# Performance work log

Measured on AMD Instinct MI355X. Metric: run time of the kernel, lower is better.

Reference implementation:

```python
import jax, jax.numpy as jnp
import numpy as np

C1, CS = 512, 32
EPS = 1e-5
_HI, _HJ = np.triu_indices(CS, k=1)  # pairwise (i<j) hadamard index pairs, cs_expand = 496


def setup_inputs() -> dict:
    key = jax.random.key(0)
    ks = jax.random.split(key, 9)
    B, H, W = 16, 32, 32
    return dict(
        x=jax.random.normal(ks[0], (B, C1, H, W), jnp.float32),
        fc_w=jax.random.normal(ks[1], (C1, C1), jnp.float32) * 0.05,   # 1x1 conv kernel
        fc_b=jax.random.normal(ks[2], (C1,), jnp.float32) * 0.05,
        bn_gamma=jax.random.normal(ks[3], (C1,), jnp.float32) * 0.1 + 1.0,
        bn_beta=jax.random.normal(ks[4], (C1,), jnp.float32) * 0.1,
        bn_mean=jax.random.normal(ks[5], (C1,), jnp.float32) * 0.1,    # BN running mean
        bn_var=jax.random.uniform(ks[6], (C1,), jnp.float32) + 0.5,    # BN running var (positive)
        eva_w=jax.random.normal(ks[7], (C1, C1), jnp.float32) * 0.05,
        eva_b=jax.random.normal(ks[8], (C1,), jnp.float32) * 0.05,
    )


def reference(x, fc_w, fc_b, bn_gamma, bn_beta, bn_mean, bn_var, eva_w, eva_b):
    hi = jnp.asarray(_HI)
    hj = jnp.asarray(_HJ)
    # 1x1 conv (pointwise GEMM over channels)
    x = jnp.einsum('bchw,oc->bohw', x, fc_w) + fc_b[None, :, None, None]
    # BatchNorm2d, eval mode (running stats)
    scale = bn_gamma / jnp.sqrt(bn_var + EPS)
    x = (x - bn_mean[None, :, None, None]) * scale[None, :, None, None] + bn_beta[None, :, None, None]
    # channel evaluation logits: global avg pool -> linear
    logits = jnp.mean(x, axis=(2, 3)) @ eva_w.T + eva_b  # [B, C1]
    # top-cs channel selection and gather (eval path)
    _, idx = jax.lax.top_k(logits, CS)                    # [B, CS]
    x_sel = jax.vmap(lambda xi, ii: xi[ii])(x, idx)       # [B, CS, H, W]
    # pairwise hadamard expansion: gather-multiply over (i<j) pairs
    prod = x_sel[:, hi] * x_sel[:, hj]                    # [B, cs_expand, H, W]
    # CrossHadaNorm: per-channel standardize with batch stats, affine from
    # cross-products of norm_x affine params gathered via hadamard_i/j
    mean = jnp.mean(prod, axis=(0, 2, 3), keepdims=True)
    var = jnp.var(prod, axis=(0, 2, 3), keepdims=True)
    g = (bn_gamma[hi] * bn_gamma[hj])[None, :, None, None]
    b = (bn_beta[hi] * bn_beta[hj])[None, :, None, None]
    prod = (prod - mean) / jnp.sqrt(var + EPS) * g + b
    return jnp.concatenate([x, prod], axis=1)             # [B, c1 + cs_expand, H, W]
```

## Files before the change

### kernel.cpp

```cpp
#include <hip/hip_runtime.h>
#include <stdint.h>
#include <stddef.h>

#define B_   16
#define C1_  512
#define HW_  1024
#define CS_  32
#define CE_  496
#define CO_  1008

typedef __attribute__((ext_vector_type(8))) short short8;
typedef __attribute__((ext_vector_type(4))) short short4v;
typedef __attribute__((ext_vector_type(4))) float f32x4;

__device__ __forceinline__ short f2bf(float f) {
  unsigned u = __builtin_bit_cast(unsigned, f);
  unsigned r = (u + 0x7fffu + ((u >> 16) & 1u)) >> 16;
  return (short)(unsigned short)r;
}

__device__ __forceinline__ void gload_lds16(const void* g, void* l) {
  __builtin_amdgcn_global_load_lds(
      (const __attribute__((address_space(1))) unsigned int*)g,
      (__attribute__((address_space(3))) unsigned int*)l, 16, 0, 0);
}

__global__ __launch_bounds__(256) void prep_kernel(
    const float* __restrict__ fc_w, const float* __restrict__ fc_b,
    const float* __restrict__ bn_gamma, const float* __restrict__ bn_beta,
    const float* __restrict__ bn_mean, const float* __restrict__ bn_var,
    short* __restrict__ wbf, float* __restrict__ bs, float* __restrict__ bb) {
  int bid = blockIdx.x, tid = threadIdx.x;
  if (bid < 1024) {
    int i = bid * 256 + tid;
    wbf[i] = f2bf(fc_w[i]);
  } else {
    for (int o = tid; o < C1_; o += 256) {
      float s = bn_gamma[o] / sqrtf(bn_var[o] + 1e-5f);
      bs[o] = s;
      bb[o] = (fc_b[o] - bn_mean[o]) * s + bn_beta[o];
    }
  }
}

__global__ __launch_bounds__(256) void transpose_pool(const float* __restrict__ x,
                                                      short* __restrict__ xT,
                                                      float* __restrict__ partial) {
  __shared__ float tile[64][65];
  int bid = blockIdx.x;
  int b = bid >> 7;
  int tt = bid & 127;
  int ct = tt >> 4, pt = tt & 15;
  int c0 = ct * 64, p0 = pt * 64;
  int tid = threadIdx.x;
  int rr = tid >> 4, lc = tid & 15;
  const float* xb = x + (size_t)b * C1_ * HW_;
#pragma unroll
  for (int it = 0; it < 4; ++it) {
    int c = it * 16 + rr;
    int p4 = lc * 4;
    float4 v = *(const float4*)(xb + (size_t)(c0 + c) * HW_ + p0 + p4);
    tile[c][p4+0] = v.x; tile[c][p4+1] = v.y; tile[c][p4+2] = v.z; tile[c][p4+3] = v.w;
    float g = v.x + v.y + v.z + v.w;
    g += __shfl_down(g, 8, 16);
    g += __shfl_down(g, 4, 16);
    g += __shfl_down(g, 2, 16);
    g += __shfl_down(g, 1, 16);
    if (lc == 0) partial[((size_t)b * 16 + pt) * C1_ + c0 + c] = g;
  }
  __syncthreads();
#pragma unroll
  for (int it = 0; it < 4; ++it) {
    int p = it * 16 + rr;
    int c4 = lc * 4;
    short4v o;
    o[0] = f2bf(tile[c4+0][p]);
    o[1] = f2bf(tile[c4+1][p]);
    o[2] = f2bf(tile[c4+2][p]);
    o[3] = f2bf(tile[c4+3][p]);
    *(short4v*)(xT + (size_t)b * HW_ * C1_ + (size_t)(p0 + p) * C1_ + c0 + c4) = o;
  }
}

__global__ __launch_bounds__(64) void fc_pool_kernel(
    const float* __restrict__ partial, const float* __restrict__ fc_w,
    const float* __restrict__ bs, const float* __restrict__ bb,
    float* __restrict__ pb) {
  int b = blockIdx.x >> 3, ot = blockIdx.x & 7;
  int tid = threadIdx.x;
  __shared__ float px[512];
  for (int c = tid; c < 512; c += 64) {
    float s = 0.f;
#pragma unroll
    for (int pt = 0; pt < 16; ++pt) s += partial[((size_t)b * 16 + pt) * C1_ + c];
    px[c] = s * (1.f / 1024.f);
  }
  __syncthreads();
  int o = ot * 64 + tid;
  const float4* wr = (const float4*)(fc_w + (size_t)o * 512);
  float acc = 0.f;
#pragma unroll 8
  for (int q = 0; q < 128; ++q) {
    float4 w = wr[q];
    acc += w.x * px[q*4] + w.y * px[q*4+1] + w.z * px[q*4+2] + w.w * px[q*4+3];
  }
  pb[b * 512 + o] = acc * bs[o] + bb[o];
}

__global__ __launch_bounds__(64) void eva_kernel(
    const float* __restrict__ pb, const float* __restrict__ eva_w,
    const float* __restrict__ eva_b, float* __restrict__ logits) {
  int b = blockIdx.x >> 3, ot = blockIdx.x & 7;
  int tid = threadIdx.x;
  __shared__ float ps[512];
  for (int c = tid; c < 512; c += 64) ps[c] = pb[b * 512 + c];
  __syncthreads();
  int o = ot * 64 + tid;
  const float4* wr = (const float4*)(eva_w + (size_t)o * 512);
  float acc = 0.f;
#pragma unroll 8
  for (int q = 0; q < 128; ++q) {
    float4 w = wr[q];
    acc += w.x * ps[q*4] + w.y * ps[q*4+1] + w.z * ps[q*4+2] + w.w * ps[q*4+3];
  }
  logits[b * 512 + o] = acc + eva_b[o];
}

__global__ __launch_bounds__(64) void topk_kernel(const float* __restrict__ logits,
                                                  int* __restrict__ idx) {
  int b = blockIdx.x, lane = threadIdx.x;
  float v[8];
  int base = lane * 8;
#pragma unroll
  for (int u = 0; u < 8; ++u) v[u] = logits[b * 512 + base + u];
  for (int it = 0; it < CS_; ++it) {
    float bv = v[0]; int bu = 0;
#pragma unroll
    for (int u = 1; u < 8; ++u) if (v[u] > bv) { bv = v[u]; bu = u; }
    int bi = base + bu;
    for (int off = 32; off; off >>= 1) {
      float ov = __shfl_down(bv, off);
      int   oi = __shfl_down(bi, off);
      if (ov > bv || (ov == bv && oi < bi)) { bv = ov; bi = oi; }
    }
    bi = __shfl(bi, 0);
    if (lane == 0) idx[b * CS_ + it] = bi;
#pragma unroll
    for (int u = 0; u < 8; ++u) if (bi == base + u) v[u] = -3.4e38f;
  }
}

__global__ __launch_bounds__(256) void gemm_kernel(const short* __restrict__ W,
                                                   const short* __restrict__ XT,
                                                   const float* __restrict__ bs,
                                                   const float* __restrict__ bb,
                                                   float* __restrict__ out) {
  __shared__ char smem[65536];
  int bid = (blockIdx.x & 7) * 64 + (blockIdx.x >> 3);
  int b = bid >> 5;
  int t = bid & 31;
  int mt = t & 3, ntile = t >> 2;
  int m0 = mt * 128, n0 = ntile * 128;
  const short* Ag = W + (size_t)m0 * 512;
  const short* Bg = XT + (size_t)b * HW_ * 512 + (size_t)n0 * 512;
  int tid = threadIdx.x;
  int lane = tid & 63, wave = tid >> 6;
  int wr = wave >> 1, wc = wave & 1;
  int mrow = wr * 64, ncol = wc * 64;
  int lrow = lane & 15;
  int swz = (lrow & 7) << 4;

  f32x4 acc[4][4];
#pragma unroll
  for (int i = 0; i < 4; ++i)
#pragma unroll
    for (int j = 0; j < 4; ++j) acc[i][j] = (f32x4){0.f, 0.f, 0.f, 0.f};

#define STAGE(dstbase, k0)                                                      \
  {                                                                             \
    _Pragma("unroll")                                                           \
    for (int it_ = 0; it_ < 4; ++it_) {                                         \
      int s_ = it_ * 256 + tid;                                                 \
      int L_ = s_ * 16;                                                         \
      int row_ = L_ >> 7;                                                       \
      int w_ = L_ & 127;                                                        \
      int srcs_ = (w_ ^ ((row_ & 7) << 4)) >> 1;                                \
      gload_lds16(Ag + (size_t)row_ * 512 + (k0) + srcs_,                       \
                  smem + (dstbase) + L_);                                       \
      gload_lds16(Bg + (size_t)row_ * 512 + (k0) + srcs_,                       \
                  smem + 32768 + (dstbase) + L_);                               \
    }                                                                           \
  }

  STAGE(0, 0)
  asm volatile("s_waitcnt vmcnt(0)" ::: "memory");
  __syncthreads();

  int cur = 0;
  for (int kt = 0; kt < 8; ++kt) {
    if (kt < 7) STAGE((cur ^ 1) * 16384, (kt + 1) * 64)
    const char* Ab = smem + cur * 16384;
    const char* Bb = smem + 32768 + cur * 16384;
#pragma unroll
    for (int kk = 0; kk < 2; ++kk) {
      int kb = (kk * 64 + (lane >> 4) * 16) ^ swz;
      short8 af[4], bfv[4];
#pragma unroll
      for (int f = 0; f < 4; ++f) {
        af[f]  = *(const short8*)(Ab + (mrow + f * 16 + lrow) * 128 + kb);
        bfv[f] = *(const short8*)(Bb + (ncol + f * 16 + lrow) * 128 + kb);
      }
#pragma unroll
      for (int mf = 0; mf < 4; ++mf)
#pragma unroll
        for (int nf = 0; nf < 4; ++nf)
          acc[mf][nf] = __builtin_amdgcn_mfma_f32_16x16x32_bf16(af[mf], bfv[nf], acc[mf][nf], 0, 0, 0);
    }
    asm volatile("s_waitcnt vmcnt(0)" ::: "memory");
    __syncthreads();
    cur ^= 1;
  }

  float* outb = out + (size_t)b * CO_ * HW_;
#pragma unroll
  for (int mf = 0; mf < 4; ++mf) {
#pragma unroll
    for (int j = 0; j < 4; ++j) {
      int o = m0 + mrow + mf * 16 + (lane >> 4) * 4 + j;
      float s = bs[o], bv = bb[o];
#pragma unroll
      for (int nf = 0; nf < 4; ++nf) {
        int p = n0 + ncol + nf * 16 + lrow;
        outb[(size_t)o * HW_ + p] = acc[mf][nf][j] * s + bv;
      }
    }
  }
#undef STAGE
}

__global__ __launch_bounds__(256) void hada_kernel(
    const int* __restrict__ idx, const float* __restrict__ bn_gamma,
    const float* __restrict__ bn_beta, float* __restrict__ out) {
  int e = blockIdx.x, tid = threadIdx.x;
  int lane = tid & 63, wave = tid >> 6;
  int i = 0, rem = e;
  while (rem >= 31 - i) { rem -= 31 - i; ++i; }
  int j = i + 1 + rem;

  __shared__ int chi[16], chj[16];
  if (tid < 16) chi[tid] = idx[tid * CS_ + i];
  else if (tid < 32) chj[tid - 16] = idx[(tid - 16) * CS_ + j];
  __syncthreads();

  f32x4 p[16];
  float s = 0.f, s2 = 0.f;
#pragma unroll
  for (int b = 0; b < 16; ++b) {
    const float4* xi = (const float4*)(out + ((size_t)b * CO_ + chi[b]) * HW_);
    const float4* xj = (const float4*)(out + ((size_t)b * CO_ + chj[b]) * HW_);
    float4 a = xi[tid], c = xj[tid];
    p[b][0] = a.x * c.x; p[b][1] = a.y * c.y; p[b][2] = a.z * c.z; p[b][3] = a.w * c.w;
    s  += p[b][0] + p[b][1] + p[b][2] + p[b][3];
    s2 += p[b][0]*p[b][0] + p[b][1]*p[b][1] + p[b][2]*p[b][2] + p[b][3]*p[b][3];
  }
  for (int off = 32; off; off >>= 1) { s += __shfl_down(s, off); s2 += __shfl_down(s2, off); }
  __shared__ float red[8];
  if (lane == 0) { red[wave] = s; red[4 + wave] = s2; }
  __syncthreads();
  float S  = red[0] + red[1] + red[2] + red[3];
  float S2 = red[4] + red[5] + red[6] + red[7];
  float mean = S * (1.f / 16384.f);
  float var  = S2 * (1.f / 16384.f) - mean * mean;
  float sc = (bn_gamma[i] * bn_gamma[j]) / sqrtf(var + 1e-5f);
  float bi_ = bn_beta[i] * bn_beta[j] - mean * sc;

#pragma unroll
  for (int b = 0; b < 16; ++b) {
    float4 r;
    r.x = p[b][0] * sc + bi_;
    r.y = p[b][1] * sc + bi_;
    r.z = p[b][2] * sc + bi_;
    r.w = p[b][3] * sc + bi_;
    ((float4*)(out + ((size_t)b * CO_ + C1_ + e) * HW_))[tid] = r;
  }
}

#define XT_OFF     ((size_t)0)
#define WBF_OFF    ((size_t)16777216)
#define PART_OFF   ((size_t)17301504)
#define PB_OFF     ((size_t)17825792)
#define LOG_OFF    ((size_t)17858560)
#define IDX_OFF    ((size_t)17891328)
#define BS_OFF     ((size_t)17893376)
#define BB_OFF     ((size_t)17895424)

extern "C" void kernel_launch(void* const* d_in, const int* in_sizes, int n_in,
                              void* d_out, int out_size, void* d_ws, size_t ws_size,
                              hipStream_t stream) {
  const float* x        = (const float*)d_in[0];
  const float* fc_w     = (const float*)d_in[1];
  const float* fc_b     = (const float*)d_in[2];
  const float* bn_gamma = (const float*)d_in[3];
  const float* bn_beta  = (const float*)d_in[4];
  const float* bn_mean  = (const float*)d_in[5];
  const float* bn_var   = (const float*)d_in[6];
  const float* eva_w    = (const float*)d_in[7];
  const float* eva_b    = (const float*)d_in[8];
  float* out = (float*)d_out;
  char* ws = (char*)d_ws;

  short* xT      = (short*)(ws + XT_OFF);
  short* wbf     = (short*)(ws + WBF_OFF);
  float* partial = (float*)(ws + PART_OFF);
  float* pb      = (float*)(ws + PB_OFF);
  float* logits  = (float*)(ws + LOG_OFF);
  int*   idx     = (int*)(ws + IDX_OFF);
  float* bs      = (float*)(ws + BS_OFF);
  float* bb      = (float*)(ws + BB_OFF);

  hipLaunchKernelGGL(prep_kernel, dim3(1025), dim3(256), 0, stream,
                     fc_w, fc_b, bn_gamma, bn_beta, bn_mean, bn_var, wbf, bs, bb);
  hipLaunchKernelGGL(transpose_pool, dim3(2048), dim3(256), 0, stream, x, xT, partial);
  hipLaunchKernelGGL(fc_pool_kernel, dim3(128), dim3(64), 0, stream,
                     partial, fc_w, bs, bb, pb);
  hipLaunchKernelGGL(eva_kernel, dim3(128), dim3(64), 0, stream,
                     pb, eva_w, eva_b, logits);
  hipLaunchKernelGGL(topk_kernel, dim3(16), dim3(64), 0, stream, logits, idx);
  hipLaunchKernelGGL(gemm_kernel, dim3(512), dim3(256), 0, stream, wbf, xT, bs, bb, out);
  hipLaunchKernelGGL(hada_kernel, dim3(CE_), dim3(256), 0, stream,
                     idx, bn_gamma, bn_beta, out);
}
```

Measured before the change: 94.97 us.

## Merge prep into transpose kernel and fuse selection stages into cooperative kernel

The weight conversion and BN-constant prep blocks are appended to the transpose/pool grid, removing one launch. The fc-pool, eva linear and top-k kernels are combined into one cooperative kernel separated by grid-wide syncs, replacing three launches with one. This cuts launch gaps between small serial kernels, at the cost of grid.sync overhead and the cooperative-launch requirements.

```diff
diff --git a/kernel.cpp b/kernel.cpp
--- a/kernel.cpp
+++ b/kernel.cpp
@@ -1,6 +1,9 @@
 #include <hip/hip_runtime.h>
+#include <hip/hip_cooperative_groups.h>
 #include <stdint.h>
 #include <stddef.h>
+
+namespace cg = cooperative_groups;
 
 #define B_   16
 #define C1_  512
@@ -25,34 +28,38 @@
       (__attribute__((address_space(3))) unsigned int*)l, 16, 0, 0);
 }
 
-__global__ __launch_bounds__(256) void prep_kernel(
-    const float* __restrict__ fc_w, const float* __restrict__ fc_b,
-    const float* __restrict__ bn_gamma, const float* __restrict__ bn_beta,
-    const float* __restrict__ bn_mean, const float* __restrict__ bn_var,
-    short* __restrict__ wbf, float* __restrict__ bs, float* __restrict__ bb) {
-  int bid = blockIdx.x, tid = threadIdx.x;
-  if (bid < 1024) {
-    int i = bid * 256 + tid;
-    wbf[i] = f2bf(fc_w[i]);
-  } else {
-    for (int o = tid; o < C1_; o += 256) {
-      float s = bn_gamma[o] / sqrtf(bn_var[o] + 1e-5f);
-      bs[o] = s;
-      bb[o] = (fc_b[o] - bn_mean[o]) * s + bn_beta[o];
-    }
-  }
-}
-
 __global__ __launch_bounds__(256) void transpose_pool(const float* __restrict__ x,
                                                       short* __restrict__ xT,
-                                                      float* __restrict__ partial) {
+                                                      float* __restrict__ partial,
+                                                      const float* __restrict__ fc_w,
+                                                      const float* __restrict__ fc_b,
+                                                      const float* __restrict__ bn_gamma,
+                                                      const float* __restrict__ bn_beta,
+                                                      const float* __restrict__ bn_mean,
+                                                      const float* __restrict__ bn_var,
+                                                      short* __restrict__ wbf,
+                                                      float* __restrict__ bs,
+                                                      float* __restrict__ bb) {
+  int bid = blockIdx.x;
+  int tid = threadIdx.x;
+  if (bid >= 2048) {
+    if (bid < 3072) {
+      int i = (bid - 2048) * 256 + tid;
+      wbf[i] = f2bf(fc_w[i]);
+    } else {
+      for (int o = tid; o < C1_; o += 256) {
+        float s = bn_gamma[o] / sqrtf(bn_var[o] + 1e-5f);
+        bs[o] = s;
+        bb[o] = (fc_b[o] - bn_mean[o]) * s + bn_beta[o];
+      }
+    }
+    return;
+  }
   __shared__ float tile[64][65];
-  int bid = blockIdx.x;
   int b = bid >> 7;
   int tt = bid & 127;
   int ct = tt >> 4, pt = tt & 15;
   int c0 = ct * 64, p0 = pt * 64;
-  int tid = threadIdx.x;
   int rr = tid >> 4, lc = tid & 15;
   const float* xb = x + (size_t)b * C1_ * HW_;
 #pragma unroll
@@ -82,71 +89,73 @@
   }
 }
 
-__global__ __launch_bounds__(64) void fc_pool_kernel(
+__global__ __launch_bounds__(64) void select_coop(
     const float* __restrict__ partial, const float* __restrict__ fc_w,
     const float* __restrict__ bs, const float* __restrict__ bb,
-    float* __restrict__ pb) {
+    const float* __restrict__ eva_w, const float* __restrict__ eva_b,
+    float* __restrict__ pb, float* __restrict__ logits, int* __restrict__ idx) {
+  cg::grid_group grid = cg::this_grid();
   int b = blockIdx.x >> 3, ot = blockIdx.x & 7;
   int tid = threadIdx.x;
-  __shared__ float px[512];
-  for (int c = tid; c < 512; c += 64) {
-    float s = 0.f;
-#pragma unroll
-    for (int pt = 0; pt < 16; ++pt) s += partial[((size_t)b * 16 + pt) * C1_ + c];
-    px[c] = s * (1.f / 1024.f);
-  }
-  __syncthreads();
-  int o = ot * 64 + tid;
-  const float4* wr = (const float4*)(fc_w + (size_t)o * 512);
-  float acc = 0.f;
+
+  {
+    __shared__ float px[512];
+    for (int c = tid; c < 512; c += 64) {
+      float s = 0.f;
+#pragma unroll
+      for (int pt = 0; pt < 16; ++pt) s += partial[((size_t)b * 16 + pt) * C1_ + c];
+      px[c] = s * (1.f / 1024.f);
+    }
+    __syncthreads();
+    int o = ot * 64 + tid;
+    const float4* wr = (const float4*)(fc_w + (size_t)o * 512);
+    float acc = 0.f;
 #pragma unroll 8
-  for (int q = 0; q < 128; ++q) {
-    float4 w = wr[q];
-    acc += w.x * px[q*4] + w.y * px[q*4+1] + w.z * px[q*4+2] + w.w * px[q*4+3];
-  }
-  pb[b * 512 + o] = acc * bs[o] + bb[o];
-}
-
-__global__ __launch_bounds__(64) void eva_kernel(
-    const float* __restrict__ pb, const float* __restrict__ eva_w,
-    const float* __restrict__ eva_b, float* __restrict__ logits) {
-  int b = blockIdx.x >> 3, ot = blockIdx.x & 7;
-  int tid = threadIdx.x;
-  __shared__ float ps[512];
-  for (int c = tid; c < 512; c += 64) ps[c] = pb[b * 512 + c];
-  __syncthreads();
-  int o = ot * 64 + tid;
-  const float4* wr = (const float4*)(eva_w + (size_t)o * 512);
-  float acc = 0.f;
+    for (int q = 0; q < 128; ++q) {
+      float4 w = wr[q];
+      acc += w.x * px[q*4] + w.y * px[q*4+1] + w.z * px[q*4+2] + w.w * px[q*4+3];
+    }
+    pb[b * 512 + o] = acc * bs[o] + bb[o];
+  }
+  grid.sync();
+
+  {
+    __shared__ float ps[512];
+    for (int c = tid; c < 512; c += 64) ps[c] = pb[b * 512 + c];
+    __syncthreads();
+    int o = ot * 64 + tid;
+    const float4* wr = (const float4*)(eva_w + (size_t)o * 512);
+    float acc = 0.f;
 #pragma unroll 8
-  for (int q = 0; q < 128; ++q) {
-    float4 w = wr[q];
-    acc += w.x * ps[q*4] + w.y * ps[q*4+1] + w.z * ps[q*4+2] + w.w * ps[q*4+3];
-  }
-  logits[b * 512 + o] = acc + eva_b[o];
-}
-
-__global__ __launch_bounds__(64) void topk_kernel(const float* __restrict__ logits,
-                                                  int* __restrict__ idx) {
-  int b = blockIdx.x, lane = threadIdx.x;
-  float v[8];
-  int base = lane * 8;
-#pragma unroll
-  for (int u = 0; u < 8; ++u) v[u] = logits[b * 512 + base + u];
-  for (int it = 0; it < CS_; ++it) {
-    float bv = v[0]; int bu = 0;
-#pragma unroll
-    for (int u = 1; u < 8; ++u) if (v[u] > bv) { bv = v[u]; bu = u; }
-    int bi = base + bu;
-    for (int off = 32; off; off >>= 1) {
-      float ov = __shfl_down(bv, off);
-      int   oi = __shfl_down(bi, off);
-      if (ov > bv || (ov == bv && oi < bi)) { bv = ov; bi = oi; }
-    }
-    bi = __shfl(bi, 0);
-    if (lane == 0) idx[b * CS_ + it] = bi;
-#pragma unroll
-    for (int u = 0; u < 8; ++u) if (bi == base + u) v[u] = -3.4e38f;
+    for (int q = 0; q < 128; ++q) {
+      float4 w = wr[q];
+      acc += w.x * ps[q*4] + w.y * ps[q*4+1] + w.z * ps[q*4+2] + w.w * ps[q*4+3];
+    }
+    logits[b * 512 + o] = acc + eva_b[o];
+  }
+  grid.sync();
+
+  if (blockIdx.x < 16) {
+    int bb_ = blockIdx.x, lane = tid;
+    float v[8];
+    int base = lane * 8;
+#pragma unroll
+    for (int u = 0; u < 8; ++u) v[u] = logits[bb_ * 512 + base + u];
+    for (int it = 0; it < CS_; ++it) {
+      float bv = v[0]; int bu = 0;
+#pragma unroll
+      for (int u = 1; u < 8; ++u) if (v[u] > bv) { bv = v[u]; bu = u; }
+      int bi = base + bu;
+      for (int off = 32; off; off >>= 1) {
+        float ov = __shfl_down(bv, off);
+        int   oi = __shfl_down(bi, off);
+        if (ov > bv || (ov == bv && oi < bi)) { bv = ov; bi = oi; }
+      }
+      bi = __shfl(bi, 0);
+      if (lane == 0) idx[bb_ * CS_ + it] = bi;
+#pragma unroll
+      for (int u = 0; u < 8; ++u) if (bi == base + u) v[u] = -3.4e38f;
+    }
   }
 }
 
@@ -318,14 +327,18 @@
   float* bs      = (float*)(ws + BS_OFF);
   float* bb      = (float*)(ws + BB_OFF);
 
-  hipLaunchKernelGGL(prep_kernel, dim3(1025), dim3(256), 0, stream,
-                     fc_w, fc_b, bn_gamma, bn_beta, bn_mean, bn_var, wbf, bs, bb);
-  hipLaunchKernelGGL(transpose_pool, dim3(2048), dim3(256), 0, stream, x, xT, partial);
-  hipLaunchKernelGGL(fc_pool_kernel, dim3(128), dim3(64), 0, stream,
-                     partial, fc_w, bs, bb, pb);
-  hipLaunchKernelGGL(eva_kernel, dim3(128), dim3(64), 0, stream,
-                     pb, eva_w, eva_b, logits);
-  hipLaunchKernelGGL(topk_kernel, dim3(16), dim3(64), 0, stream, logits, idx);
+  hipLaunchKernelGGL(transpose_pool, dim3(3073), dim3(256), 0, stream,
+                     x, xT, partial, fc_w, fc_b, bn_gamma, bn_beta, bn_mean, bn_var,
+                     wbf, bs, bb);
+
+  {
+    void* args[9] = {(void*)&partial, (void*)&fc_w, (void*)&bs, (void*)&bb,
+                     (void*)&eva_w, (void*)&eva_b, (void*)&pb, (void*)&logits,
+                     (void*)&idx};
+    hipLaunchCooperativeKernel((const void*)select_coop, dim3(128), dim3(64),
+                               args, 0, stream);
+  }
+
   hipLaunchKernelGGL(gemm_kernel, dim3(512), dim3(256), 0, stream, wbf, xT, bs, bb, out);
   hipLaunchKernelGGL(hada_kernel, dim3(CE_), dim3(256), 0, stream,
                      idx, bn_gamma, bn_beta, out);
```

Result: slower. 121.6 us (+28.0%).

## Fuse transpose/bf16 conversion and pooling into GEMM reading fp32 x directly

Applied to the files above, without the earlier changes.

Removes the separate transpose_pool kernel and its bf16 xT workspace. The GEMM now streams fp32 x tiles (channel-major) into swizzled LDS, converts them to bf16 while building the MFMA B fragments, and computes the spatial pooling partial sums in the mt==0 blocks. It also moves to a 3-buffer, K=32 software pipeline with split vmcnt waits. This saves a full read/write pass over x, at the cost of scalar LDS reads and conversion work inside the inner loop, plus an extra pooling load on one quarter of the blocks.

```diff
diff --git a/kernel.cpp b/kernel.cpp
--- a/kernel.cpp
+++ b/kernel.cpp
@@ -1,4 +1,5 @@
 #include <hip/hip_runtime.h>
+#include <hip/hip_bf16.h>
 #include <stdint.h>
 #include <stddef.h>
 
@@ -10,7 +11,6 @@
 #define CO_  1008
 
 typedef __attribute__((ext_vector_type(8))) short short8;
-typedef __attribute__((ext_vector_type(4))) short short4v;
 typedef __attribute__((ext_vector_type(4))) float f32x4;
 
 __device__ __forceinline__ short f2bf(float f) {
@@ -43,43 +43,132 @@
   }
 }
 
-__global__ __launch_bounds__(256) void transpose_pool(const float* __restrict__ x,
-                                                      short* __restrict__ xT,
-                                                      float* __restrict__ partial) {
-  __shared__ float tile[64][65];
-  int bid = blockIdx.x;
-  int b = bid >> 7;
-  int tt = bid & 127;
-  int ct = tt >> 4, pt = tt & 15;
-  int c0 = ct * 64, p0 = pt * 64;
+__global__ __launch_bounds__(256) void gemm_kernel(const short* __restrict__ W,
+                                                   const float* __restrict__ X,
+                                                   const float* __restrict__ bs,
+                                                   const float* __restrict__ bb,
+                                                   float* __restrict__ out,
+                                                   float* __restrict__ partial) {
+  __shared__ char smem[73728];
+  __shared__ float pool_lds[512];
+  int bid = (blockIdx.x & 7) * 64 + (blockIdx.x >> 3);
+  int b = bid >> 5;
+  int t = bid & 31;
+  int mt = t & 3, ntile = t >> 2;
+  int m0 = mt * 128, n0 = ntile * 128;
+  const short* Ag = W + (size_t)m0 * 512;
+  const float* Xb = X + (size_t)b * C1_ * HW_;
   int tid = threadIdx.x;
-  int rr = tid >> 4, lc = tid & 15;
-  const float* xb = x + (size_t)b * C1_ * HW_;
-#pragma unroll
-  for (int it = 0; it < 4; ++it) {
-    int c = it * 16 + rr;
-    int p4 = lc * 4;
-    float4 v = *(const float4*)(xb + (size_t)(c0 + c) * HW_ + p0 + p4);
-    tile[c][p4+0] = v.x; tile[c][p4+1] = v.y; tile[c][p4+2] = v.z; tile[c][p4+3] = v.w;
-    float g = v.x + v.y + v.z + v.w;
-    g += __shfl_down(g, 8, 16);
-    g += __shfl_down(g, 4, 16);
-    g += __shfl_down(g, 2, 16);
-    g += __shfl_down(g, 1, 16);
-    if (lc == 0) partial[((size_t)b * 16 + pt) * C1_ + c0 + c] = g;
-  }
-  __syncthreads();
-#pragma unroll
-  for (int it = 0; it < 4; ++it) {
-    int p = it * 16 + rr;
-    int c4 = lc * 4;
-    short4v o;
-    o[0] = f2bf(tile[c4+0][p]);
-    o[1] = f2bf(tile[c4+1][p]);
-    o[2] = f2bf(tile[c4+2][p]);
-    o[3] = f2bf(tile[c4+3][p]);
-    *(short4v*)(xT + (size_t)b * HW_ * C1_ + (size_t)(p0 + p) * C1_ + c0 + c4) = o;
-  }
+  int lane = tid & 63, wave = tid >> 6;
+  int wr = wave >> 1, wc = wave & 1;
+  int mrow = wr * 64, ncol = wc * 64;
+  int lrow = lane & 15;
+  int slotA = lane >> 4;
+
+  f32x4 acc[4][4];
+#pragma unroll
+  for (int i = 0; i < 4; ++i)
+#pragma unroll
+    for (int j = 0; j < 4; ++j) acc[i][j] = (f32x4){0.f, 0.f, 0.f, 0.f};
+
+#define STAGE(bufidx, kt_)                                                      \
+  {                                                                             \
+    int k0_ = (kt_) * 32;                                                       \
+    _Pragma("unroll")                                                           \
+    for (int it_ = 0; it_ < 2; ++it_) {                                         \
+      int L_ = (it_ * 256 + tid) * 16;                                          \
+      int row_ = L_ >> 6;                                                       \
+      int srcb_ = (L_ & 63) ^ (((row_ >> 1) & 3) << 4);                         \
+      gload_lds16(Ag + (size_t)row_ * 512 + k0_ + (srcb_ >> 1),                 \
+                  smem + (bufidx) * 8192 + L_);                                 \
+    }                                                                           \
+    _Pragma("unroll")                                                           \
+    for (int it_ = 0; it_ < 4; ++it_) {                                         \
+      int L_ = (it_ * 256 + tid) * 16;                                          \
+      int c_ = L_ >> 9;                                                         \
+      int sl_ = (L_ >> 4) & 31;                                                 \
+      int sp_ = sl_ ^ (c_ & 7) ^ ((c_ >> 2) & 6);                               \
+      gload_lds16(Xb + (size_t)(k0_ + c_) * HW_ + n0 + sp_ * 4,                 \
+                  smem + 24576 + (bufidx) * 16384 + L_);                        \
+    }                                                                           \
+  }
+
+#define STEP(KT, VN)                                                            \
+  {                                                                             \
+    asm volatile("s_waitcnt vmcnt(" #VN ")" ::: "memory");                      \
+    __builtin_amdgcn_s_barrier();                                               \
+    if ((KT) + 2 < 16) STAGE(((KT) + 2) % 3, (KT) + 2)                          \
+    const char* Ab = smem + ((KT) % 3) * 8192;                                  \
+    const char* Bb = smem + 24576 + ((KT) % 3) * 16384;                         \
+    short8 af[4], bfv[4];                                                       \
+    _Pragma("unroll")                                                           \
+    for (int f = 0; f < 4; ++f) {                                               \
+      int rowA = mrow + f * 16 + lrow;                                          \
+      af[f] = *(const short8*)(Ab + rowA * 64 + ((slotA ^ ((rowA >> 1) & 3)) << 4)); \
+    }                                                                           \
+    _Pragma("unroll")                                                           \
+    for (int f = 0; f < 4; ++f) {                                               \
+      int p_ = ncol + f * 16 + lrow;                                            \
+      int ps_ = p_ >> 2, pw_ = (p_ & 3) * 4;                                    \
+      short8 bv_;                                                               \
+      _Pragma("unroll")                                                         \
+      for (int u = 0; u < 8; ++u) {                                             \
+        int c_ = slotA * 8 + u;                                                 \
+        float fv_ = *(const float*)(Bb + c_ * 512 +                             \
+                     ((ps_ ^ (c_ & 7) ^ ((c_ >> 2) & 6)) << 4) + pw_);          \
+        bv_[u] = f2bf(fv_);                                                     \
+      }                                                                         \
+      bfv[f] = bv_;                                                             \
+    }                                                                           \
+    if (mt == 0) {                                                              \
+      int c2_ = tid >> 3, j_ = tid & 7;                                         \
+      const f32x4* pr_ = (const f32x4*)(Bb + c2_ * 512 + j_ * 64);              \
+      f32x4 q0_ = pr_[0], q1_ = pr_[1], q2_ = pr_[2], q3_ = pr_[3];             \
+      float g_ = (q0_[0]+q0_[1]+q0_[2]+q0_[3]) + (q1_[0]+q1_[1]+q1_[2]+q1_[3])  \
+               + (q2_[0]+q2_[1]+q2_[2]+q2_[3]) + (q3_[0]+q3_[1]+q3_[2]+q3_[3]); \
+      g_ += __shfl_down(g_, 4, 8);                                              \
+      g_ += __shfl_down(g_, 2, 8);                                              \
+      g_ += __shfl_down(g_, 1, 8);                                              \
+      if (j_ == 0) pool_lds[(KT) * 32 + c2_] = g_;                              \
+    }                                                                           \
+    _Pragma("unroll")                                                           \
+    for (int mf = 0; mf < 4; ++mf)                                              \
+      _Pragma("unroll")                                                         \
+      for (int nf = 0; nf < 4; ++nf)                                            \
+        acc[mf][nf] = __builtin_amdgcn_mfma_f32_16x16x32_bf16(af[mf], bfv[nf],  \
+                                                              acc[mf][nf], 0, 0, 0); \
+  }
+
+  STAGE(0, 0)
+  STAGE(1, 1)
+
+  STEP(0, 6)  STEP(1, 6)  STEP(2, 6)  STEP(3, 6)
+  STEP(4, 6)  STEP(5, 6)  STEP(6, 6)  STEP(7, 6)
+  STEP(8, 6)  STEP(9, 6)  STEP(10, 6) STEP(11, 6)
+  STEP(12, 6) STEP(13, 6) STEP(14, 6) STEP(15, 0)
+
+  if (mt == 0) {
+    __syncthreads();
+    partial[((size_t)b * 8 + ntile) * 512 + tid]       = pool_lds[tid];
+    partial[((size_t)b * 8 + ntile) * 512 + 256 + tid] = pool_lds[256 + tid];
+  }
+
+  float* outb = out + (size_t)b * CO_ * HW_;
+#pragma unroll
+  for (int mf = 0; mf < 4; ++mf) {
+#pragma unroll
+    for (int j = 0; j < 4; ++j) {
+      int o = m0 + mrow + mf * 16 + (lane >> 4) * 4 + j;
+      float s = bs[o], bv = bb[o];
+#pragma unroll
+      for (int nf = 0; nf < 4; ++nf) {
+        int p = n0 + ncol + nf * 16 + lrow;
+        outb[(size_t)o * HW_ + p] = acc[mf][nf][j] * s + bv;
+      }
+    }
+  }
+#undef STEP
+#undef STAGE
 }
 
 __global__ __launch_bounds__(64) void fc_pool_kernel(
@@ -92,7 +181,7 @@
   for (int c = tid; c < 512; c += 64) {
     float s = 0.f;
 #pragma unroll
-    for (int pt = 0; pt < 16; ++pt) s += partial[((size_t)b * 16 + pt) * C1_ + c];
+    for (int pn = 0; pn < 8; ++pn) s += partial[((size_t)b * 8 + pn) * 512 + c];
     px[c] = s * (1.f / 1024.f);
   }
   __syncthreads();
@@ -150,94 +239,6 @@
   }
 }
 
-__global__ __launch_bounds__(256) void gemm_kernel(const short* __restrict__ W,
-                                                   const short* __restrict__ XT,
-                                                   const float* __restrict__ bs,
-                                                   const float* __restrict__ bb,
-                                                   float* __restrict__ out) {
-  __shared__ char smem[65536];
-  int bid = (blockIdx.x & 7) * 64 + (blockIdx.x >> 3);
-  int b = bid >> 5;
-  int t = bid & 31;
-  int mt = t & 3, ntile = t >> 2;
-  int m0 = mt * 128, n0 = ntile * 128;
-  const short* Ag = W + (size_t)m0 * 512;
-  const short* Bg = XT + (size_t)b * HW_ * 512 + (size_t)n0 * 512;
-  int tid = threadIdx.x;
-  int lane = tid & 63, wave = tid >> 6;
-  int wr = wave >> 1, wc = wave & 1;
-  int mrow = wr * 64, ncol = wc * 64;
-  int lrow = lane & 15;
-  int swz = (lrow & 7) << 4;
-
-  f32x4 acc[4][4];
-#pragma unroll
-  for (int i = 0; i < 4; ++i)
-#pragma unroll
-    for (int j = 0; j < 4; ++j) acc[i][j] = (f32x4){0.f, 0.f, 0.f, 0.f};
-
-#define STAGE(dstbase, k0)                                                      \
-  {                                                                             \
-    _Pragma("unroll")                                                           \
-    for (int it_ = 0; it_ < 4; ++it_) {                                         \
-      int s_ = it_ * 256 + tid;                                                 \
-      int L_ = s_ * 16;                                                         \
-      int row_ = L_ >> 7;                                                       \
-      int w_ = L_ & 127;                                                        \
-      int srcs_ = (w_ ^ ((row_ & 7) << 4)) >> 1;                                \
-      gload_lds16(Ag + (size_t)row_ * 512 + (k0) + srcs_,                       \
-                  smem + (dstbase) + L_);                                       \
-      gload_lds16(Bg + (size_t)row_ * 512 + (k0) + srcs_,                       \
-                  smem + 32768 + (dstbase) + L_);                               \
-    }                                                                           \
-  }
-
-  STAGE(0, 0)
-  asm volatile("s_waitcnt vmcnt(0)" ::: "memory");
-  __syncthreads();
-
-  int cur = 0;
-  for (int kt = 0; kt < 8; ++kt) {
-    if (kt < 7) STAGE((cur ^ 1) * 16384, (kt + 1) * 64)
-    const char* Ab = smem + cur * 16384;
-    const char* Bb = smem + 32768 + cur * 16384;
-#pragma unroll
-    for (int kk = 0; kk < 2; ++kk) {
-      int kb = (kk * 64 + (lane >> 4) * 16) ^ swz;
-      short8 af[4], bfv[4];
-#pragma unroll
-      for (int f = 0; f < 4; ++f) {
-        af[f]  = *(const short8*)(Ab + (mrow + f * 16 + lrow) * 128 + kb);
-        bfv[f] = *(const short8*)(Bb + (ncol + f * 16 + lrow) * 128 + kb);
-      }
-#pragma unroll
-      for (int mf = 0; mf < 4; ++mf)
-#pragma unroll
-        for (int nf = 0; nf < 4; ++nf)
-          acc[mf][nf] = __builtin_amdgcn_mfma_f32_16x16x32_bf16(af[mf], bfv[nf], acc[mf][nf], 0, 0, 0);
-    }
-    asm volatile("s_waitcnt vmcnt(0)" ::: "memory");
-    __syncthreads();
-    cur ^= 1;
-  }
-
-  float* outb = out + (size_t)b * CO_ * HW_;
-#pragma unroll
-  for (int mf = 0; mf < 4; ++mf) {
-#pragma unroll
-    for (int j = 0; j < 4; ++j) {
-      int o = m0 + mrow + mf * 16 + (lane >> 4) * 4 + j;
-      float s = bs[o], bv = bb[o];
-#pragma unroll
-      for (int nf = 0; nf < 4; ++nf) {
-        int p = n0 + ncol + nf * 16 + lrow;
-        outb[(size_t)o * HW_ + p] = acc[mf][nf][j] * s + bv;
-      }
-    }
-  }
-#undef STAGE
-}
-
 __global__ __launch_bounds__(256) void hada_kernel(
     const int* __restrict__ idx, const float* __restrict__ bn_gamma,
     const float* __restrict__ bn_beta, float* __restrict__ out) {
@@ -285,14 +286,13 @@
   }
 }
 
-#define XT_OFF     ((size_t)0)
-#define WBF_OFF    ((size_t)16777216)
-#define PART_OFF   ((size_t)17301504)
-#define PB_OFF     ((size_t)17825792)
-#define LOG_OFF    ((size_t)17858560)
-#define IDX_OFF    ((size_t)17891328)
-#define BS_OFF     ((size_t)17893376)
-#define BB_OFF     ((size_t)17895424)
+#define WBF_OFF    ((size_t)0)
+#define PART_OFF   ((size_t)524288)
+#define PB_OFF     ((size_t)786432)
+#define LOG_OFF    ((size_t)819200)
+#define IDX_OFF    ((size_t)851968)
+#define BS_OFF     ((size_t)854016)
+#define BB_OFF     ((size_t)856064)
 
 extern "C" void kernel_launch(void* const* d_in, const int* in_sizes, int n_in,
                               void* d_out, int out_size, void* d_ws, size_t ws_size,
@@ -309,7 +309,6 @@
   float* out = (float*)d_out;
   char* ws = (char*)d_ws;
 
-  short* xT      = (short*)(ws + XT_OFF);
   short* wbf     = (short*)(ws + WBF_OFF);
   float* partial = (float*)(ws + PART_OFF);
   float* pb      = (float*)(ws + PB_OFF);
@@ -320,13 +319,13 @@
 
   hipLaunchKernelGGL(prep_kernel, dim3(1025), dim3(256), 0, stream,
                      fc_w, fc_b, bn_gamma, bn_beta, bn_mean, bn_var, wbf, bs, bb);
-  hipLaunchKernelGGL(transpose_pool, dim3(2048), dim3(256), 0, stream, x, xT, partial);
+  hipLaunchKernelGGL(gemm_kernel, dim3(512), dim3(256), 0, stream,
+                     wbf, x, bs, bb, out, partial);
   hipLaunchKernelGGL(fc_pool_kernel, dim3(128), dim3(64), 0, stream,
                      partial, fc_w, bs, bb, pb);
   hipLaunchKernelGGL(eva_kernel, dim3(128), dim3(64), 0, stream,
                      pb, eva_w, eva_b, logits);
   hipLaunchKernelGGL(topk_kernel, dim3(16), dim3(64), 0, stream, logits, idx);
-  hipLaunchKernelGGL(gemm_kernel, dim3(512), dim3(256), 0, stream, wbf, xT, bs, bb, out);
   hipLaunchKernelGGL(hada_kernel, dim3(CE_), dim3(256), 0, stream,
                      idx, bn_gamma, bn_beta, out);
 }
```

Measured after the change: 97.08 us. +2.2%, slower.
